# Performance work log

Measured on AMD Instinct MI355X. Metric: run time of the kernel, lower is better.

## Reference

```python
import jax, jax.numpy as jnp
import numpy as np

B, T, D, H = 128, 1024, 256, 256


def setup_inputs() -> dict:
    key = jax.random.key(0)
    ks = jax.random.split(key, 6)
    s_i = 1.0 / np.sqrt(D).astype(np.float32)
    s_h = 1.0 / np.sqrt(H).astype(np.float32)
    obs = jax.random.normal(ks[0], (B, T, D), jnp.float32)
    done = jax.random.randint(ks[1], (B, T), 0, 2).astype(bool)
    init_hstate = jax.random.normal(ks[2], (B, H), jnp.float32)
    # GRU params (flax GRUCell layout): input dense has bias, hidden r/z dense no bias, hidden n dense has bias
    Wi = jax.random.normal(ks[3], (D, 3 * H), jnp.float32) * s_i      # [ir | iz | in]
    bi = jnp.zeros((3 * H,), jnp.float32)
    Wh_rz = jax.random.normal(ks[4], (H, 2 * H), jnp.float32) * s_h   # [hr | hz]
    Wh_n = jax.random.normal(ks[5], (H, H), jnp.float32) * s_h
    bh_n = jnp.zeros((H,), jnp.float32)
    return dict(obs=obs, done=done, init_hstate=init_hstate,
                Wi=Wi, bi=bi, Wh_rz=Wh_rz, Wh_n=Wh_n, bh_n=bh_n)


def reference(obs, done, init_hstate, Wi, bi, Wh_rz, Wh_n, bh_n):
    Hn = Wh_n.shape[0]
    # Precompute all input projections in one big GEMM (same math as per-step dense_i)
    x_proj = obs @ Wi + bi                      # [B, T, 3H]
    x_t = jnp.swapaxes(x_proj, 0, 1)            # [T, B, 3H]
    d_t = jnp.swapaxes(done, 0, 1)              # [T, B]

    def step(h, inp):
        xp, d = inp
        # reset carry to initialize_carry (zeros) where episode is done
        h = jnp.where(d[:, None], 0.0, h)
        hr_hz = h @ Wh_rz                        # [B, 2H]
        r = jax.nn.sigmoid(xp[:, :Hn] + hr_hz[:, :Hn])
        z = jax.nn.sigmoid(xp[:, Hn:2 * Hn] + hr_hz[:, Hn:])
        n = jnp.tanh(xp[:, 2 * Hn:] + r * (h @ Wh_n + bh_n))
        h_new = (1.0 - z) * n + z * h
        return h_new, h_new

    final_h, ys = jax.lax.scan(step, init_hstate, (x_t, d_t))
    return final_h, jnp.swapaxes(ys, 0, 1)      # carry, outputs [B, T, H]
```

## Files before the change

kernel.cpp:

```cpp
#include <hip/hip_runtime.h>
#include <hip/hip_bf16.h>
#include <hip/hip_fp16.h>


#define B_ 128
#define T_ 1024
#define D_ 256
#define H_ 256
#define CHUNKS_ 32
#define CHUNK_T_ (T_ / CHUNKS_)

typedef _Float16 half2v __attribute__((ext_vector_type(2)));
typedef _Float16 half8v __attribute__((ext_vector_type(8)));
typedef float f32x4 __attribute__((ext_vector_type(4)));

__global__ __launch_bounds__(256, 2) void xproj_gemm(
    const float* __restrict__ A,
    const float* __restrict__ W,
    const float* __restrict__ bias,
    _Float16* __restrict__ C)
{
  constexpr int LDS_K = 40;
  __shared__ __align__(16) _Float16 As[128 * LDS_K];
  __shared__ __align__(16) _Float16 Bs[128 * LDS_K];
  const int m0 = blockIdx.x * 128;
  const int n0 = blockIdx.y * 128;
  const int tid = threadIdx.x;
  const int lane = tid & 63;
  const int wv = tid >> 6;
  const int wm = (wv >> 1) * 64;
  const int wn = (wv & 1) * 64;
  const int q = lane >> 4;
  const int lm = lane & 15;

  f32x4 acc[4][4];
#pragma unroll
  for (int i = 0; i < 4; ++i)
#pragma unroll
    for (int j = 0; j < 4; ++j)
      acc[i][j] = (f32x4){0.f, 0.f, 0.f, 0.f};

  const int ar = tid >> 1, ac = (tid & 1) * 16;
  const int bk = tid >> 3, bj = (tid & 7) * 16;

  for (int k0 = 0; k0 < 256; k0 += 32) {
    const float* ap = A + (size_t)(m0 + ar) * 256 + k0 + ac;
    float4 a0 = *(const float4*)(ap + 0);
    float4 a1 = *(const float4*)(ap + 4);
    float4 a2 = *(const float4*)(ap + 8);
    float4 a3 = *(const float4*)(ap + 12);
    const float* bp = W + (size_t)(k0 + bk) * 768 + n0 + bj;
    float4 b0 = *(const float4*)(bp + 0);
    float4 b1 = *(const float4*)(bp + 4);
    float4 b2 = *(const float4*)(bp + 8);
    float4 b3 = *(const float4*)(bp + 12);

    _Float16 av[16];
    av[0] = (_Float16)a0.x; av[1] = (_Float16)a0.y; av[2] = (_Float16)a0.z; av[3] = (_Float16)a0.w;
    av[4] = (_Float16)a1.x; av[5] = (_Float16)a1.y; av[6] = (_Float16)a1.z; av[7] = (_Float16)a1.w;
    av[8] = (_Float16)a2.x; av[9] = (_Float16)a2.y; av[10] = (_Float16)a2.z; av[11] = (_Float16)a2.w;
    av[12] = (_Float16)a3.x; av[13] = (_Float16)a3.y; av[14] = (_Float16)a3.z; av[15] = (_Float16)a3.w;
    *(int4*)&As[ar * LDS_K + ac] = *(int4*)&av[0];
    *(int4*)&As[ar * LDS_K + ac + 8] = *(int4*)&av[8];

    _Float16 bvv[16];
    bvv[0] = (_Float16)b0.x; bvv[1] = (_Float16)b0.y; bvv[2] = (_Float16)b0.z; bvv[3] = (_Float16)b0.w;
    bvv[4] = (_Float16)b1.x; bvv[5] = (_Float16)b1.y; bvv[6] = (_Float16)b1.z; bvv[7] = (_Float16)b1.w;
    bvv[8] = (_Float16)b2.x; bvv[9] = (_Float16)b2.y; bvv[10] = (_Float16)b2.z; bvv[11] = (_Float16)b2.w;
    bvv[12] = (_Float16)b3.x; bvv[13] = (_Float16)b3.y; bvv[14] = (_Float16)b3.z; bvv[15] = (_Float16)b3.w;
#pragma unroll
    for (int i = 0; i < 16; ++i) Bs[(bj + i) * LDS_K + bk] = bvv[i];
    __syncthreads();

    half8v af[4], bfr[4];
#pragma unroll
    for (int i = 0; i < 4; ++i)
      af[i] = *(const half8v*)&As[(wm + i * 16 + lm) * LDS_K + q * 8];
#pragma unroll
    for (int j = 0; j < 4; ++j)
      bfr[j] = *(const half8v*)&Bs[(wn + j * 16 + lm) * LDS_K + q * 8];
#pragma unroll
    for (int i = 0; i < 4; ++i)
#pragma unroll
      for (int j = 0; j < 4; ++j)
        acc[i][j] = __builtin_amdgcn_mfma_f32_16x16x32_f16(af[i], bfr[j], acc[i][j], 0, 0, 0);
    __syncthreads();
  }

#pragma unroll
  for (int j = 0; j < 4; ++j) {
    const int n = n0 + wn + j * 16 + lm;
    const float bv = bias[n];
#pragma unroll
    for (int i = 0; i < 4; ++i) {
#pragma unroll
      for (int r = 0; r < 4; ++r) {
        const int m = m0 + wm + i * 16 + q * 4 + r;
        C[(size_t)m * 768 + n] = (_Float16)(acc[i][j][r] + bv);
      }
    }
  }
}


__device__ __forceinline__ int swzb(int row, int colbyte) {
  return row * 512 + (colbyte ^ ((row & 7) << 4));
}

__device__ __forceinline__ int xswz(int row, int colbyte) {
  return row * 1536 + (colbyte ^ ((row & 7) << 4));
}

__device__ __forceinline__ void load16_to_lds(const void* g, void* l) {
  __builtin_amdgcn_global_load_lds(
      (const __attribute__((address_space(1))) unsigned int*)g,
      (__attribute__((address_space(3))) unsigned int*)l, 16, 0, 0);
}

__global__ __launch_bounds__(256, 1) void gru_scan_mfma(
    const _Float16* __restrict__ xp,
    const int* __restrict__ done,
    const float* __restrict__ h0,
    const float* __restrict__ Wh_rz,
    const float* __restrict__ Wh_n,
    const float* __restrict__ bh_n,
    float* __restrict__ out_final,
    float* __restrict__ out_ys)
{
  const int bx = blockIdx.x;
  const int grp = bx & 7;
  const int chunk = bx >> 3;
  const int t0 = chunk * CHUNK_T_;
  const int tend = t0 + CHUNK_T_;
  const int tid = threadIdx.x;
  const int w = tid >> 6;
  const int l = tid & 63;
  const int lm = l & 15;
  const int q = l >> 4;
  const int colb = w * 64 + lm;

  __shared__ __align__(16) _Float16 h_lds[2][16 * 256];
  __shared__ __align__(16) _Float16 xp_lds[2][16 * 768];

  half8v bf[3][4][8];
#pragma unroll
  for (int ro = 0; ro < 3; ++ro)
#pragma unroll
    for (int cg = 0; cg < 4; ++cg) {
#pragma unroll
      for (int kc = 0; kc < 8; ++kc) {
        half8v v;
#pragma unroll
        for (int j = 0; j < 8; ++j) {
          const int k = kc * 32 + q * 8 + j;
          const int c = colb + cg * 16;
          const float wv = (ro < 2) ? Wh_rz[(size_t)k * 512 + ro * 256 + c]
                                    : Wh_n[(size_t)k * 256 + c];
          v[j] = (_Float16)wv;
        }
        bf[ro][cg][kc] = v;
      }
      __builtin_amdgcn_sched_barrier(0);
    }

  float bhn[4];
#pragma unroll
  for (int cg = 0; cg < 4; ++cg) bhn[cg] = bh_n[colb + cg * 16];

  unsigned xsrc[6];
#pragma unroll
  for (int j = 0; j < 6; ++j) {
    const int c = w * 384 + j * 64 + l;
    const int row = c / 96;
    const int pc = c - row * 96;
    const int lc = pc ^ (row & 7);
    xsrc[j] = (unsigned)((grp * 16 + row) * T_ + t0) * 1536u + (unsigned)lc * 16u;
  }

  unsigned doff[4];
  unsigned yoff[4];
  int dcur[4];
#pragma unroll
  for (int r = 0; r < 4; ++r) {
    const int b = grp * 16 + q * 4 + r;
    doff[r] = (unsigned)(b * T_ + t0) * 4u;
    yoff[r] = (unsigned)(b * T_ + t0) * (unsigned)(H_ * 4);
    dcur[r] = *(const int*)((const char*)done + doff[r]);
  }

  char* hR = (char*)&h_lds[0][0];
  char* hW = (char*)&h_lds[1][0];
#pragma unroll
  for (int cg = 0; cg < 4; ++cg)
#pragma unroll
    for (int r = 0; r < 4; ++r) {
      const int row = q * 4 + r;
      const int c = colb + cg * 16;
      float v = 0.f;
      if (chunk == 0) {
        const int b = grp * 16 + row;
        v = done[(size_t)b * T_] ? 0.f : h0[(size_t)b * H_ + c];
      }
      *(_Float16*)(hR + swzb(row, c * 2)) = (_Float16)v;
    }

  {
    char* xb = (char*)&xp_lds[t0 & 1][0] + w * 6144;
#pragma unroll
    for (int j = 0; j < 6; ++j)
      load16_to_lds((const char*)xp + xsrc[j], xb + j * 1024);
#pragma unroll
    for (int j = 0; j < 6; ++j) xsrc[j] += 1536u;
  }
  __syncthreads();

  unsigned act = (chunk == 0) ? 0xFu : 0u;
  unsigned endm = 0u;

  for (int t = t0;;) {
#pragma unroll
    for (int r = 0; r < 4; ++r)
      if (dcur[r]) {
        if (t >= tend) endm |= (1u << r);
        else           act  |= (1u << r);
      }
    if (t >= T_) break;
    if (__all(endm == 0xFu)) break;

    const bool hasnext = (t + 1 < T_);

    int dn[4];
#pragma unroll
    for (int r = 0; r < 4; ++r) {
      const int v = *(const int*)((const char*)done + doff[r] + (hasnext ? 4 : 0));
      dn[r] = hasnext ? v : 0;
    }

    if (hasnext) {
      char* xb = (char*)&xp_lds[(t + 1) & 1][0] + w * 6144;
#pragma unroll
      for (int j = 0; j < 6; ++j)
        load16_to_lds((const char*)xp + xsrc[j], xb + j * 1024);
    }
#pragma unroll
    for (int j = 0; j < 6; ++j) xsrc[j] += 1536u;

    const char* xq = (const char*)&xp_lds[t & 1][0];

    half8v a[8];
#pragma unroll
    for (int kc = 0; kc < 8; ++kc)
      a[kc] = *(const half8v*)(hR + swzb(lm, kc * 64 + q * 16));

#pragma unroll
    for (int hf = 0; hf < 2; ++hf) {
      f32x4 acc[3][2];
#pragma unroll
      for (int c2 = 0; c2 < 2; ++c2) {
        const int col = colb + (hf * 2 + c2) * 16;
#pragma unroll
        for (int r = 0; r < 4; ++r) {
          const int row = q * 4 + r;
          acc[0][c2][r] = (float)*(const _Float16*)(xq + xswz(row, col * 2));
          acc[1][c2][r] = (float)*(const _Float16*)(xq + xswz(row, (col + 256) * 2));
          acc[2][c2][r] = bhn[hf * 2 + c2];
        }
      }

#pragma unroll
      for (int kc = 0; kc < 8; ++kc)
#pragma unroll
        for (int ro = 0; ro < 3; ++ro)
#pragma unroll
          for (int c2 = 0; c2 < 2; ++c2)
            acc[ro][c2] = __builtin_amdgcn_mfma_f32_16x16x32_f16(
                a[kc], bf[ro][hf * 2 + c2][kc], acc[ro][c2], 0, 0, 0);

#pragma unroll
      for (int c2 = 0; c2 < 2; ++c2) {
        const int col = colb + (hf * 2 + c2) * 16;
#pragma unroll
        for (int r = 0; r < 4; ++r) {
          const int row = q * 4 + r;
          const float xn = (float)*(const _Float16*)(xq + xswz(row, (col + 512) * 2));
          const float hm = (float)*(const _Float16*)(hR + swzb(row, col * 2));
          const float rr = 1.f / (1.f + __expf(-acc[0][c2][r]));
          const float zz = 1.f / (1.f + __expf(-acc[1][c2][r]));
          const float npre = xn + rr * acc[2][c2][r];
          const float e = __expf(-2.f * fabsf(npre));
          const float tv = (1.f - e) / (1.f + e);
          const float nn = npre < 0.f ? -tv : tv;
          const float hnew = (1.f - zz) * nn + zz * hm;
          *(_Float16*)(hW + swzb(row, col * 2)) =
              (_Float16)(dn[r] ? 0.f : hnew);
          if (((act >> r) & 1u) && !((endm >> r) & 1u)) {
            *(float*)((char*)out_ys + yoff[r] + (unsigned)col * 4u) = hnew;
            if (t == T_ - 1)
              out_final[(size_t)(grp * 16 + row) * H_ + col] = hnew;
          }
        }
      }
    }

#pragma unroll
    for (int r = 0; r < 4; ++r) {
      doff[r] += 4u;
      yoff[r] += (unsigned)(H_ * 4);
      dcur[r] = dn[r];
    }
    { char* tmp = hR; hR = hW; hW = tmp; }
    ++t;
    __syncthreads();
  }
}

extern "C" void kernel_launch(void* const* d_in, const int* in_sizes, int n_in,
                              void* d_out, int out_size, void* d_ws, size_t ws_size,
                              hipStream_t stream) {
  const float* obs   = (const float*)d_in[0];
  const int*   done  = (const int*)d_in[1];
  const float* h0    = (const float*)d_in[2];
  const float* Wi    = (const float*)d_in[3];
  const float* bi    = (const float*)d_in[4];
  const float* Wh_rz = (const float*)d_in[5];
  const float* Wh_n  = (const float*)d_in[6];
  const float* bh_n  = (const float*)d_in[7];
  float* out = (float*)d_out;
  _Float16* xp = (_Float16*)d_ws;

  xproj_gemm<<<dim3(1024, 6), 256, 0, stream>>>(obs, Wi, bi, xp);
  gru_scan_mfma<<<dim3(256), 256, 0, stream>>>(xp, done, h0, Wh_rz, Wh_n, bh_n,
                                               out, out + B_ * H_);
}
```

Before: 869.4 us.

## Split GRU scan columns across eight waves with 512-thread blocks

Doubles the scan kernel's block size from 256 to 512 threads, so each of eight waves owns 32 hidden columns instead of 64. This halves the per-wave MFMA chain and register-resident weight fragments on each serial timestep, which shortens the critical path of the recurrence. The A fragments are now loaded per k-chunk inside the loop rather than all up front, and the output offset is derived from the done offset to free registers. The cost is more waves sharing each barrier per step and smaller per-wave loads of the input projection into LDS.

```diff
diff --git a/kernel.cpp b/kernel.cpp
--- a/kernel.cpp
+++ b/kernel.cpp
@@ -117,7 +117,7 @@
       (__attribute__((address_space(3))) unsigned int*)l, 16, 0, 0);
 }
 
-__global__ __launch_bounds__(256, 1) void gru_scan_mfma(
+__global__ __launch_bounds__(512, 2) void gru_scan_mfma(
     const _Float16* __restrict__ xp,
     const int* __restrict__ done,
     const float* __restrict__ h0,
@@ -137,16 +137,16 @@
   const int l = tid & 63;
   const int lm = l & 15;
   const int q = l >> 4;
-  const int colb = w * 64 + lm;
+  const int colb = w * 32 + lm;
 
   __shared__ __align__(16) _Float16 h_lds[2][16 * 256];
   __shared__ __align__(16) _Float16 xp_lds[2][16 * 768];
 
-  half8v bf[3][4][8];
+  half8v bf[3][2][8];
 #pragma unroll
   for (int ro = 0; ro < 3; ++ro)
 #pragma unroll
-    for (int cg = 0; cg < 4; ++cg) {
+    for (int cg = 0; cg < 2; ++cg) {
 #pragma unroll
       for (int kc = 0; kc < 8; ++kc) {
         half8v v;
@@ -163,14 +163,14 @@
       __builtin_amdgcn_sched_barrier(0);
     }
 
-  float bhn[4];
-#pragma unroll
-  for (int cg = 0; cg < 4; ++cg) bhn[cg] = bh_n[colb + cg * 16];
-
-  unsigned xsrc[6];
-#pragma unroll
-  for (int j = 0; j < 6; ++j) {
-    const int c = w * 384 + j * 64 + l;
+  float bhn[2];
+#pragma unroll
+  for (int cg = 0; cg < 2; ++cg) bhn[cg] = bh_n[colb + cg * 16];
+
+  unsigned xsrc[3];
+#pragma unroll
+  for (int j = 0; j < 3; ++j) {
+    const int c = w * 192 + j * 64 + l;
     const int row = c / 96;
     const int pc = c - row * 96;
     const int lc = pc ^ (row & 7);
@@ -178,20 +178,18 @@
   }
 
   unsigned doff[4];
-  unsigned yoff[4];
   int dcur[4];
 #pragma unroll
   for (int r = 0; r < 4; ++r) {
     const int b = grp * 16 + q * 4 + r;
     doff[r] = (unsigned)(b * T_ + t0) * 4u;
-    yoff[r] = (unsigned)(b * T_ + t0) * (unsigned)(H_ * 4);
     dcur[r] = *(const int*)((const char*)done + doff[r]);
   }
 
   char* hR = (char*)&h_lds[0][0];
   char* hW = (char*)&h_lds[1][0];
 #pragma unroll
-  for (int cg = 0; cg < 4; ++cg)
+  for (int cg = 0; cg < 2; ++cg)
 #pragma unroll
     for (int r = 0; r < 4; ++r) {
       const int row = q * 4 + r;
@@ -205,12 +203,12 @@
     }
 
   {
-    char* xb = (char*)&xp_lds[t0 & 1][0] + w * 6144;
-#pragma unroll
-    for (int j = 0; j < 6; ++j)
+    char* xb = (char*)&xp_lds[t0 & 1][0] + w * 3072;
+#pragma unroll
+    for (int j = 0; j < 3; ++j)
       load16_to_lds((const char*)xp + xsrc[j], xb + j * 1024);
 #pragma unroll
-    for (int j = 0; j < 6; ++j) xsrc[j] += 1536u;
+    for (int j = 0; j < 3; ++j) xsrc[j] += 1536u;
   }
   __syncthreads();
 
@@ -237,67 +235,61 @@
     }
 
     if (hasnext) {
-      char* xb = (char*)&xp_lds[(t + 1) & 1][0] + w * 6144;
-#pragma unroll
-      for (int j = 0; j < 6; ++j)
+      char* xb = (char*)&xp_lds[(t + 1) & 1][0] + w * 3072;
+#pragma unroll
+      for (int j = 0; j < 3; ++j)
         load16_to_lds((const char*)xp + xsrc[j], xb + j * 1024);
     }
 #pragma unroll
-    for (int j = 0; j < 6; ++j) xsrc[j] += 1536u;
+    for (int j = 0; j < 3; ++j) xsrc[j] += 1536u;
 
     const char* xq = (const char*)&xp_lds[t & 1][0];
 
-    half8v a[8];
-#pragma unroll
-    for (int kc = 0; kc < 8; ++kc)
-      a[kc] = *(const half8v*)(hR + swzb(lm, kc * 64 + q * 16));
-
-#pragma unroll
-    for (int hf = 0; hf < 2; ++hf) {
-      f32x4 acc[3][2];
-#pragma unroll
-      for (int c2 = 0; c2 < 2; ++c2) {
-        const int col = colb + (hf * 2 + c2) * 16;
-#pragma unroll
-        for (int r = 0; r < 4; ++r) {
-          const int row = q * 4 + r;
-          acc[0][c2][r] = (float)*(const _Float16*)(xq + xswz(row, col * 2));
-          acc[1][c2][r] = (float)*(const _Float16*)(xq + xswz(row, (col + 256) * 2));
-          acc[2][c2][r] = bhn[hf * 2 + c2];
-        }
-      }
-
-#pragma unroll
-      for (int kc = 0; kc < 8; ++kc)
-#pragma unroll
-        for (int ro = 0; ro < 3; ++ro)
-#pragma unroll
-          for (int c2 = 0; c2 < 2; ++c2)
-            acc[ro][c2] = __builtin_amdgcn_mfma_f32_16x16x32_f16(
-                a[kc], bf[ro][hf * 2 + c2][kc], acc[ro][c2], 0, 0, 0);
-
-#pragma unroll
-      for (int c2 = 0; c2 < 2; ++c2) {
-        const int col = colb + (hf * 2 + c2) * 16;
-#pragma unroll
-        for (int r = 0; r < 4; ++r) {
-          const int row = q * 4 + r;
-          const float xn = (float)*(const _Float16*)(xq + xswz(row, (col + 512) * 2));
-          const float hm = (float)*(const _Float16*)(hR + swzb(row, col * 2));
-          const float rr = 1.f / (1.f + __expf(-acc[0][c2][r]));
-          const float zz = 1.f / (1.f + __expf(-acc[1][c2][r]));
-          const float npre = xn + rr * acc[2][c2][r];
-          const float e = __expf(-2.f * fabsf(npre));
-          const float tv = (1.f - e) / (1.f + e);
-          const float nn = npre < 0.f ? -tv : tv;
-          const float hnew = (1.f - zz) * nn + zz * hm;
-          *(_Float16*)(hW + swzb(row, col * 2)) =
-              (_Float16)(dn[r] ? 0.f : hnew);
-          if (((act >> r) & 1u) && !((endm >> r) & 1u)) {
-            *(float*)((char*)out_ys + yoff[r] + (unsigned)col * 4u) = hnew;
-            if (t == T_ - 1)
-              out_final[(size_t)(grp * 16 + row) * H_ + col] = hnew;
-          }
+    f32x4 acc[3][2];
+#pragma unroll
+    for (int cg = 0; cg < 2; ++cg) {
+      const int col = colb + cg * 16;
+#pragma unroll
+      for (int r = 0; r < 4; ++r) {
+        const int row = q * 4 + r;
+        acc[0][cg][r] = (float)*(const _Float16*)(xq + xswz(row, col * 2));
+        acc[1][cg][r] = (float)*(const _Float16*)(xq + xswz(row, (col + 256) * 2));
+        acc[2][cg][r] = bhn[cg];
+      }
+    }
+
+#pragma unroll
+    for (int kc = 0; kc < 8; ++kc) {
+      const half8v av = *(const half8v*)(hR + swzb(lm, kc * 64 + q * 16));
+#pragma unroll
+      for (int ro = 0; ro < 3; ++ro)
+#pragma unroll
+        for (int cg = 0; cg < 2; ++cg)
+          acc[ro][cg] = __builtin_amdgcn_mfma_f32_16x16x32_f16(
+              av, bf[ro][cg][kc], acc[ro][cg], 0, 0, 0);
+    }
+
+#pragma unroll
+    for (int cg = 0; cg < 2; ++cg) {
+      const int col = colb + cg * 16;
+#pragma unroll
+      for (int r = 0; r < 4; ++r) {
+        const int row = q * 4 + r;
+        const float xn = (float)*(const _Float16*)(xq + xswz(row, (col + 512) * 2));
+        const float hm = (float)*(const _Float16*)(hR + swzb(row, col * 2));
+        const float rr = 1.f / (1.f + __expf(-acc[0][cg][r]));
+        const float zz = 1.f / (1.f + __expf(-acc[1][cg][r]));
+        const float npre = xn + rr * acc[2][cg][r];
+        const float e = __expf(-2.f * fabsf(npre));
+        const float tv = (1.f - e) / (1.f + e);
+        const float nn = npre < 0.f ? -tv : tv;
+        const float hnew = (1.f - zz) * nn + zz * hm;
+        *(_Float16*)(hW + swzb(row, col * 2)) =
+            (_Float16)(dn[r] ? 0.f : hnew);
+        if (((act >> r) & 1u) && !((endm >> r) & 1u)) {
+          *(float*)((char*)out_ys + ((size_t)doff[r] << 8) + (unsigned)col * 4u) = hnew;
+          if (t == T_ - 1)
+            out_final[(size_t)(grp * 16 + row) * H_ + col] = hnew;
         }
       }
     }
@@ -305,7 +297,6 @@
 #pragma unroll
     for (int r = 0; r < 4; ++r) {
       doff[r] += 4u;
-      yoff[r] += (unsigned)(H_ * 4);
       dcur[r] = dn[r];
     }
     { char* tmp = hR; hR = hW; hW = tmp; }
@@ -329,6 +320,6 @@
   _Float16* xp = (_Float16*)d_ws;
 
   xproj_gemm<<<dim3(1024, 6), 256, 0, stream>>>(obs, Wi, bi, xp);
-  gru_scan_mfma<<<dim3(256), 256, 0, stream>>>(xp, done, h0, Wh_rz, Wh_n, bh_n,
+  gru_scan_mfma<<<dim3(256), 512, 0, stream>>>(xp, done, h0, Wh_rz, Wh_n, bh_n,
                                                out, out + B_ * H_);
 }
```

Measured after the change: 918.1 us. 5.6% more time.
